# Kernel tuning notes

Measured on AMD Instinct MI355X. Metric: run time of the kernel, lower is better.

## Reference

```python
import jax, jax.numpy as jnp
import numpy as np

DIM = 1024
HEADS = 8
KV_HEADS = 1
GROUPS = HEADS // KV_HEADS
D_QK = 128
D_V = 192
DIM_PAIRWISE = 128
SCALE = 64 ** -0.5  # module uses dim_head=64 for scale, not dim_head_qk
SOFTCLAMP = 5.0
RMS_EPS = 1.1920929e-07  # torch nn.RMSNorm default eps = float32 machine eps
BN_EPS = 1e-05


def setup_inputs() -> dict:
    key = jax.random.key(0)
    ks = jax.random.split(key, 12)
    b, n, i = 1, 2048, 512
    qkv_out = HEADS * D_QK + D_QK + D_V  # 1344
    inv = lambda fan_in: 1.0 / np.sqrt(fan_in)
    return {
        "x": jax.random.normal(ks[0], (b, n, DIM), jnp.float32),
        "pairwise": jax.random.normal(ks[1], (b, i, i, DIM_PAIRWISE), jnp.float32),
        "rotary_emb": jax.random.normal(ks[2], (n, D_QK), jnp.float32),
        "W_qkv": jax.random.normal(ks[3], (DIM, qkv_out), jnp.float32) * inv(DIM),
        "q_norm_w": jnp.ones((D_QK,), jnp.float32),
        "k_norm_w": jnp.ones((D_QK,), jnp.float32),
        "v_norm_w": jnp.ones((D_V,), jnp.float32),
        "bn_gamma": jax.random.normal(ks[4], (DIM_PAIRWISE,), jnp.float32) * 0.02,
        "bn_beta": jax.random.normal(ks[5], (DIM_PAIRWISE,), jnp.float32) * 0.02,
        "bn_running_var": jnp.ones((DIM_PAIRWISE,), jnp.float32),
        "W_bias": jax.random.normal(ks[6], (DIM_PAIRWISE, HEADS), jnp.float32) * inv(DIM_PAIRWISE),
        "W_out": jax.random.normal(ks[7], (HEADS * D_V, DIM), jnp.float32) * inv(HEADS * D_V),
    }


def _rmsnorm(t, w):
    var = jnp.mean(jnp.square(t), axis=-1, keepdims=True)
    return t * jax.lax.rsqrt(var + RMS_EPS) * w


def _rotate_half(t):
    t1, t2 = jnp.split(t, 2, axis=-1)
    return jnp.concatenate((-t2, t1), axis=-1)


def _apply_rope(pos, t):
    return t * jnp.cos(pos) + _rotate_half(t) * jnp.sin(pos)


def reference(x, pairwise, rotary_emb, W_qkv, q_norm_w, k_norm_w, v_norm_w,
              bn_gamma, bn_beta, bn_running_var, W_bias, W_out):
    b, n, _ = x.shape
    qkv = x @ W_qkv
    q, k, v = jnp.split(qkv, [HEADS * D_QK, HEADS * D_QK + D_QK], axis=-1)

    # q: b n (g h d) -> b g h n d ; k,v: b n (h d) -> b h n d
    q = q.reshape(b, n, GROUPS, KV_HEADS, D_QK).transpose(0, 2, 3, 1, 4)
    k = k.reshape(b, n, KV_HEADS, D_QK).transpose(0, 2, 1, 3)
    v = v.reshape(b, n, KV_HEADS, D_V).transpose(0, 2, 1, 3)

    q = _rmsnorm(q, q_norm_w) * SCALE
    k = _rmsnorm(k, k_norm_w)
    v = _rmsnorm(v, v_norm_w)

    q = _apply_rope(rotary_emb, q)
    k = _apply_rope(rotary_emb, k)

    sim = jnp.einsum('bghid,bhjd->bghij', q, k)

    # pairwise attn bias: BatchRMSNorm (eval) -> GELU -> Linear -> b g h i j
    std = jnp.sqrt(jnp.clip(bn_running_var, BN_EPS, None))
    pw = pairwise / std * (DIM_PAIRWISE ** 0.5)
    pw = pw * (bn_gamma + 1.0) + bn_beta
    pw = jax.nn.gelu(pw, approximate=False)
    attn_bias = pw @ W_bias  # [b, i, j, heads]
    bi = attn_bias.shape[1]
    attn_bias = attn_bias.reshape(b, bi, bi, GROUPS, KV_HEADS).transpose(0, 3, 4, 1, 2)

    r = n // bi  # expand_factor
    attn_bias = jnp.repeat(jnp.repeat(attn_bias, r, axis=-2), r, axis=-1)

    sim = jnp.tanh((sim + attn_bias) / SOFTCLAMP) * SOFTCLAMP
    attn = jax.nn.softmax(sim, axis=-1)

    out = jnp.einsum('bghij,bhjd->bghid', attn, v)
    out = out.transpose(0, 3, 1, 2, 4).reshape(b, n, GROUPS * KV_HEADS * D_V)
    return out @ W_out
```

## Files before the change

kernel.cpp:

```cpp
#include <hip/hip_runtime.h>
#include <math.h>

typedef unsigned short u16;
typedef __attribute__((ext_vector_type(4))) float f32x4;
typedef __attribute__((ext_vector_type(8))) short s16x8;
typedef __attribute__((ext_vector_type(8))) _Float16 f16x8;

__device__ __forceinline__ u16 f2bf(float f){
  unsigned u = __builtin_bit_cast(unsigned, f);
  u += 0x7fffu + ((u >> 16) & 1u);
  return (u16)(u >> 16);
}
__device__ __forceinline__ float bf2f(u16 h){
  unsigned u = ((unsigned)h) << 16;
  return __builtin_bit_cast(float, u);
}
__device__ __forceinline__ u16 f2h(float f){
  return __builtin_bit_cast(u16, (_Float16)f);
}
__device__ __forceinline__ float h2f(u16 h){
  return (float)__builtin_bit_cast(_Float16, h);
}
__device__ __forceinline__ f32x4 mfma16(s16x8 a, s16x8 b, f32x4 c){
  return __builtin_amdgcn_mfma_f32_16x16x32_bf16(a, b, c, 0, 0, 0);
}
__device__ __forceinline__ f32x4 mfma16h(f16x8 a, f16x8 b, f32x4 c){
  return __builtin_amdgcn_mfma_f32_16x16x32_f16(a, b, c, 0, 0, 0);
}
__device__ __forceinline__ void gload16(const void* src, const u16* ldsbase){
  __builtin_amdgcn_global_load_lds(
      (const __attribute__((address_space(1))) void*)src,
      (__attribute__((address_space(3))) void*)ldsbase, 16, 0, 0);
}

__global__ __launch_bounds__(256) void k_pre(const float* __restrict__ x,
    const float* __restrict__ Wq, const float* __restrict__ Wo,
    u16* __restrict__ Afq, u16* __restrict__ Bq1, u16* __restrict__ Bq2){
  __shared__ float tile[64][65];
  int b = blockIdx.x, t = threadIdx.x;
  if (b < 1024){
    int id = b*256 + t;
    int row = id>>7, k0 = (id&127)*8;
    const float4* xp = (const float4*)(x + (size_t)row*1024 + k0);
    float4 v0 = xp[0], v1 = xp[1];
    float vv[8] = {v0.x,v0.y,v0.z,v0.w, v1.x,v1.y,v1.z,v1.w};
    u16 hh[8];
    #pragma unroll
    for (int e=0; e<8; ++e) hh[e] = f2h(vv[e]);
    int mt = row>>7, ms = (row>>4)&7, m16 = row&15;
    int kt = k0>>6, ks2 = (k0>>5)&1, lg = (k0>>3)&3;
    int lane = lg*16 + m16;
    size_t base = (size_t)(mt*16 + kt)*8192;
    *(uint4*)&Afq[base + (size_t)(ks2*8 + ms)*512 + lane*8] = *(uint4*)hh;
    return;
  }
  const float* in; u16* Bfq; int N, nKt, nt, kt;
  if (b < 1360){
    int bb = b - 1024; nt = bb % 21; kt = bb / 21;
    in = Wq; Bfq = Bq1; N = 1344; nKt = 16;
  } else {
    int bb = b - 1360; nt = bb % 16; kt = bb / 16;
    in = Wo; Bfq = Bq2; N = 1024; nKt = 24;
  }
  #pragma unroll
  for (int i=0; i<16; ++i){
    int idx = i*256 + t;
    int r = idx>>6, c = idx&63;
    tile[r][c] = in[(size_t)(kt*64 + r)*N + nt*64 + c];
  }
  __syncthreads();
  size_t base = (size_t)(nt*nKt + kt)*4096;
  #pragma unroll
  for (int j=0; j<2; ++j){
    int idx = j*256 + t;
    int np = idx>>3, ko = idx&7;
    u16 hh[8];
    #pragma unroll
    for (int e=0; e<8; ++e) hh[e] = f2h(tile[ko*8+e][np]);
    int ks2 = ko>>2, lg = ko&3, ns = np>>4, n16 = np&15;
    int lane = lg*16 + n16;
    *(uint4*)&Bfq[base + (size_t)(ks2*4 + ns)*512 + lane*8] = *(uint4*)hh;
  }
}

__global__ __launch_bounds__(256,3) void k_g1b(const u16* __restrict__ Afq,
    const u16* __restrict__ Bq1, u16* __restrict__ qkvh,
    const float* __restrict__ pw, const float* __restrict__ rv,
    const float* __restrict__ gamma, const float* __restrict__ beta,
    const float* __restrict__ Wb, float* __restrict__ bias){
  __shared__ u16 lds[24576];
  int b = blockIdx.x, t = threadIdx.x;
  int w = t>>6, lane = t&63, lg = lane>>4, lr = lane&15;
  if (b < 336){
    int id2 = (b & 7)*42 + (b >> 3);
    int by = id2 / 21, bx = id2 - by*21;
    int iw = w&1, jw = w>>1;
    int n0 = bx*64, m0 = by*128;
    const char* srcA = (const char*)(Afq + (size_t)by*16*8192);
    const char* srcB = (const char*)(Bq1 + (size_t)bx*16*4096);
    int wb = w*1024 + lane*16;
    auto stage = [&](int kt, int cur){
      const char* ta = srcA + (size_t)kt*16384;
      const char* tb = srcB + (size_t)kt*8192;
      int ab = cur*12288;
      #pragma unroll
      for (int i=0; i<4; ++i)
        gload16(ta + i*4096 + wb, &lds[ab + ((i*4096 + w*1024)>>1)]);
      #pragma unroll
      for (int i=0; i<2; ++i)
        gload16(tb + i*4096 + wb, &lds[ab + 8192 + ((i*4096 + w*1024)>>1)]);
    };
    f32x4 acc[4][2] = {};
    stage(0, 0);
    __syncthreads();
    int cur = 0;
    for (int kt=0; kt<16; ++kt){
      if (kt+1 < 16) stage(kt+1, cur^1);
      int ab = cur*12288;
      #pragma unroll
      for (int ks2=0; ks2<2; ++ks2){
        f16x8 ah[4], bh[2];
        #pragma unroll
        for (int m=0; m<4; ++m)
          ah[m] = *(const f16x8*)&lds[ab + (size_t)(ks2*8 + iw*4 + m)*512 + lane*8];
        #pragma unroll
        for (int n=0; n<2; ++n)
          bh[n] = *(const f16x8*)&lds[ab + 8192 + (size_t)(ks2*4 + jw*2 + n)*512 + lane*8];
        #pragma unroll
        for (int m=0; m<4; ++m)
          #pragma unroll
          for (int n=0; n<2; ++n)
            acc[m][n] = mfma16h(ah[m], bh[n], acc[m][n]);
      }
      __syncthreads();
      cur ^= 1;
    }
    #pragma unroll
    for (int m=0; m<4; ++m)
      #pragma unroll
      for (int n=0; n<2; ++n)
        #pragma unroll
        for (int r=0; r<4; ++r){
          int row = m0 + iw*64 + m*16 + lg*4 + r;
          int col = n0 + jw*32 + n*16 + lr;
          qkvh[(size_t)row*1344 + col] = f2h(acc[m][n][r]);
        }
    return;
  }
  int bb = b - 336;
  float* As = (float*)lds;
  float* Bs = As + 128;
  if (t < 128){
    As[t] = 11.313708498984761f * rsqrtf(fmaxf(rv[t], 1e-5f)) * (gamma[t] + 1.0f);
    Bs[t] = beta[t];
  }
  __syncthreads();
  s16x8 wbh[4], wbl[4];
  #pragma unroll
  for (int ks=0; ks<4; ++ks){
    s16x8 vh, vl;
    #pragma unroll
    for (int e=0; e<8; ++e){
      float v = (lr < 8) ? Wb[(ks*32 + lg*8 + e)*8 + lr] : 0.0f;
      u16 hh = f2bf(v);
      vh[e] = (short)hh;
      vl[e] = (short)f2bf(v - bf2f(hh));
    }
    wbh[ks] = vh; wbl[ks] = vl;
  }
  #pragma unroll
  for (int it=0; it<2; ++it){
    int p0 = bb*128 + it*64 + w*16;
    const float* rowp = pw + (size_t)(p0 + lr)*128;
    f32x4 acc = {0.f,0.f,0.f,0.f};
    #pragma unroll
    for (int ks=0; ks<4; ++ks){
      int c = ks*32 + lg*8;
      float4 x0 = *(const float4*)(rowp + c);
      float4 x1 = *(const float4*)(rowp + c + 4);
      float4 a0 = *(const float4*)&As[c], a1 = *(const float4*)&As[c+4];
      float4 b0 = *(const float4*)&Bs[c], b1 = *(const float4*)&Bs[c+4];
      float xv[8] = {x0.x*a0.x+b0.x, x0.y*a0.y+b0.y, x0.z*a0.z+b0.z, x0.w*a0.w+b0.w,
                     x1.x*a1.x+b1.x, x1.y*a1.y+b1.y, x1.z*a1.z+b1.z, x1.w*a1.w+b1.w};
      s16x8 gh, gl;
      #pragma unroll
      for (int e=0; e<8; ++e){
        float v = xv[e];
        float z = v * 0.7071067811865476f;
        float s = fabsf(z);
        float tt = 1.0f / (1.0f + 0.3275911f*s);
        float poly = ((((1.061405429f*tt - 1.453152027f)*tt + 1.421413741f)*tt - 0.284496736f)*tt + 0.254829592f)*tt;
        float E = __expf(-s*s);
        float Q = 0.5f*v*poly*E;
        float ge = (v >= 0.0f) ? (v - Q) : Q;
        u16 hh = f2bf(ge);
        gh[e] = (short)hh;
        gl[e] = (short)f2bf(ge - bf2f(hh));
      }
      acc = mfma16(gh, wbh[ks], acc);
      acc = mfma16(gh, wbl[ks], acc);
      acc = mfma16(gl, wbh[ks], acc);
    }
    if (lr < 8)
      #pragma unroll
      for (int r=0; r<4; ++r)
        bias[(size_t)(p0 + lg*4 + r)*8 + lr] = acc[r];
  }
}

__global__ __launch_bounds__(256) void k_norm(const u16* __restrict__ qkvh,
   const float* __restrict__ rot, const float* __restrict__ qw, const float* __restrict__ kw,
   const float* __restrict__ vw, u16* __restrict__ Qf, u16* __restrict__ KVF){
  int t = threadIdx.x;
  int w = t>>6, l = t&63;
  int task = blockIdx.x*4 + w;
  int n = task/10, g = task - (task/10)*10;
  const u16* row = qkvh + (size_t)n*1344;
  size_t tbase = (size_t)(n>>5)*10240;
  if (g < 9){
    float e0 = h2f(row[g*128 + l]);
    float e1 = h2f(row[g*128 + 64 + l]);
    float s = e0*e0 + e1*e1;
    #pragma unroll
    for (int m=1; m<64; m<<=1) s += __shfl_xor(s, m, 64);
    float rr = rsqrtf(s*(1.0f/128.0f) + 1.1920929e-07f);
    const float* ww = (g < 8) ? qw : kw;
    float sc = (g < 8) ? 0.125f : 1.0f;
    float qn0 = e0*rr*ww[l]*sc;
    float qn1 = e1*rr*ww[64+l]*sc;
    float p0 = rot[(size_t)n*128 + l], p1 = rot[(size_t)n*128 + 64 + l];
    float c0, s0, c1, s1;
    __sincosf(p0, &s0, &c0);
    __sincosf(p1, &s1, &c1);
    float o0 = qn0*c0 - qn1*s0;
    float o1 = qn1*c1 + qn0*s1;
    if (g < 8){
      Qf[((size_t)g*2048 + n)*128 + l]      = f2h(o0);
      Qf[((size_t)g*2048 + n)*128 + 64 + l] = f2h(o1);
    } else {
      int d0 = l, d1 = 64 + l;
      size_t ka0 = tbase + (size_t)((d0>>5)*2 + ((n>>4)&1))*512
                 + (size_t)(((d0>>3)&3)*16 + (n&15))*8 + (d0&7);
      size_t ka1 = tbase + (size_t)((d1>>5)*2 + ((n>>4)&1))*512
                 + (size_t)(((d1>>3)&3)*16 + (n&15))*8 + (d1&7);
      KVF[ka0] = f2h(o0);
      KVF[ka1] = f2h(o1);
    }
  } else {
    float v0 = h2f(row[1152 + l]);
    float v1 = h2f(row[1152 + 64 + l]);
    float v2 = h2f(row[1152 + 128 + l]);
    float s = v0*v0 + v1*v1 + v2*v2;
    #pragma unroll
    for (int m=1; m<64; m<<=1) s += __shfl_xor(s, m, 64);
    float rr = rsqrtf(s*(1.0f/192.0f) + 1.1920929e-07f);
    int lgv = (n>>3)&3, ev = n&7;
    size_t vbase = tbase + 4096;
    float vals[3] = {v0, v1, v2};
    #pragma unroll
    for (int j=0; j<3; ++j){
      int d = j*64 + l;
      KVF[vbase + (size_t)(d>>4)*512 + (size_t)(lgv*16 + (d&15))*8 + ev]
          = f2h(vals[j]*rr*vw[d]);
    }
  }
}

__global__ __launch_bounds__(256,3) void k_gemm2(const u16* __restrict__ Afq,
    const u16* __restrict__ Bfq, void* __restrict__ Cv, int N, int nKt, int halfOut, int NX){
  __shared__ u16 lds[24576];
  int id = blockIdx.x;
  int per = gridDim.x >> 3;
  int id2 = (id & 7)*per + (id >> 3);
  int by = id2 / NX;
  int bx = id2 - by*NX;
  int t = threadIdx.x;
  int w = t>>6, lane = t&63, lg = lane>>4, lr = lane&15;
  int iw = w&1, jw = w>>1;
  int n0 = bx*64, m0 = by*128;
  const char* srcA = (const char*)(Afq + (size_t)by*nKt*8192);
  const char* srcB = (const char*)(Bfq + (size_t)bx*nKt*4096);
  int wb = w*1024 + lane*16;
  auto stage = [&](int kt, int cur){
    const char* ta = srcA + (size_t)kt*16384;
    const char* tb = srcB + (size_t)kt*8192;
    int ab = cur*12288;
    #pragma unroll
    for (int i=0; i<4; ++i)
      gload16(ta + i*4096 + wb, &lds[ab + ((i*4096 + w*1024)>>1)]);
    #pragma unroll
    for (int i=0; i<2; ++i)
      gload16(tb + i*4096 + wb, &lds[ab + 8192 + ((i*4096 + w*1024)>>1)]);
  };
  f32x4 acc[4][2] = {};
  stage(0, 0);
  __syncthreads();
  int cur = 0;
  for (int kt=0; kt<nKt; ++kt){
    if (kt+1 < nKt) stage(kt+1, cur^1);
    int ab = cur*12288;
    #pragma unroll
    for (int ks2=0; ks2<2; ++ks2){
      f16x8 ah[4], bh[2];
      #pragma unroll
      for (int m=0; m<4; ++m)
        ah[m] = *(const f16x8*)&lds[ab + (size_t)(ks2*8 + iw*4 + m)*512 + lane*8];
      #pragma unroll
      for (int n=0; n<2; ++n)
        bh[n] = *(const f16x8*)&lds[ab + 8192 + (size_t)(ks2*4 + jw*2 + n)*512 + lane*8];
      #pragma unroll
      for (int m=0; m<4; ++m)
        #pragma unroll
        for (int n=0; n<2; ++n)
          acc[m][n] = mfma16h(ah[m], bh[n], acc[m][n]);
    }
    __syncthreads();
    cur ^= 1;
  }
  #pragma unroll
  for (int m=0; m<4; ++m)
    #pragma unroll
    for (int n=0; n<2; ++n)
      #pragma unroll
      for (int r=0; r<4; ++r){
        int row = m0 + iw*64 + m*16 + lg*4 + r;
        int col = n0 + jw*32 + n*16 + lr;
        if (halfOut) ((u16*)Cv)[(size_t)row*N + col] = f2h(acc[m][n][r]);
        else         ((float*)Cv)[(size_t)row*N + col] = acc[m][n][r];
      }
}

__global__ __launch_bounds__(256,2) void k_attn6(const u16* __restrict__ Qf,
  const u16* __restrict__ KVF, const float* __restrict__ bias,
  u16* __restrict__ OP, float* __restrict__ SP){
  __shared__ u16 lds[24576];
  int t = threadIdx.x;
  int w = t>>6, lane = t&63, lg = lane>>4, lr = lane&15;
  int q0 = blockIdx.x*32;
  int h  = blockIdx.y*4 + w;
  int zi = blockIdx.z;
  f16x8 qf[2][4];
  #pragma unroll
  for (int qi=0; qi<2; ++qi){
    const u16* qb = Qf + ((size_t)h*2048 + q0 + qi*16 + lr)*128 + lg*8;
    #pragma unroll
    for (int ks=0; ks<4; ++ks) qf[qi][ks] = *(const f16x8*)(qb + ks*32);
  }
  const char* kvb = (const char*)KVF + (size_t)zi*16*20480;
  int wb = w*1024 + lane*16;
  auto stage = [&](int jt, int cur){
    const char* src = kvb + (size_t)jt*20480;
    gload16(src + wb,         &lds[cur*4096 + (w*1024>>1)]);
    gload16(src + 4096 + wb,  &lds[cur*4096 + 2048 + (w*1024>>1)]);
    gload16(src + 8192 + wb,  &lds[8192 + cur*6144 + (w*1024>>1)]);
    gload16(src + 12288 + wb, &lds[8192 + cur*6144 + 2048 + (w*1024>>1)]);
    gload16(src + 16384 + wb, &lds[8192 + cur*6144 + 4096 + (w*1024>>1)]);
  };
  float bCur[2][2], bNxt[2][2];
  auto loadBias = [&](int jt, float bb[2][2]){
    int jq = (zi*512 + jt*32)>>2;
    #pragma unroll
    for (int qi=0; qi<2; ++qi)
      #pragma unroll
      for (int kj=0; kj<2; ++kj)
        bb[qi][kj] = bias[((size_t)((q0>>2) + qi*4 + lg)*512 + jq + kj*4 + (lr>>2))*8 + h];
  };
  stage(0, 0);
  loadBias(0, bCur);
  __syncthreads();
  f32x4 accO[2][12] = {};
  f32x4 accR[2] = {};
  f16x8 vone;
  #pragma unroll
  for (int e=0; e<8; ++e) vone[e] = (_Float16)1.0f;
  int psb = 20480 + w*1024;
  int po0 = lane*8;       po0 ^= ((po0>>6)&7)<<3;
  int po1 = 512 + lane*8; po1 ^= ((po1>>6)&7)<<3;
  int cur = 0;
  for (int jt=0; jt<16; ++jt){
    if (jt < 15){ stage(jt+1, cur^1); loadBias(jt+1, bNxt); }
    f32x4 accS[2][2] = {};
    #pragma unroll
    for (int ks=0; ks<4; ++ks){
      #pragma unroll
      for (int kj=0; kj<2; ++kj){
        f16x8 kb = *(const f16x8*)&lds[cur*4096 + (ks*2+kj)*512 + lane*8];
        accS[0][kj] = mfma16h(qf[0][ks], kb, accS[0][kj]);
        accS[1][kj] = mfma16h(qf[1][ks], kb, accS[1][kj]);
      }
    }
    #pragma unroll
    for (int qi=0; qi<2; ++qi)
      #pragma unroll
      for (int kj=0; kj<2; ++kj){
        float bv = bCur[qi][kj];
        #pragma unroll
        for (int r=0; r<4; ++r){
          float s = accS[qi][kj][r] + bv;
          float te = __expf(0.4f*s);
          float ri; asm("v_rcp_f32 %0, %1" : "=v"(ri) : "v"(te + 1.0f));
          float p = __expf(-10.0f*ri);
          int o = qi*512 + ((kj*2 + (lr>>3))*16 + lg*4 + r)*8 + (lr&7);
          o ^= ((o>>6)&7)<<3;
          lds[psb + o] = f2h(p);
        }
      }
    f16x8 pa0 = *(const f16x8*)&lds[psb + po0];
    f16x8 pa1 = *(const f16x8*)&lds[psb + po1];
    #pragma unroll
    for (int df=0; df<12; ++df){
      f16x8 vb = *(const f16x8*)&lds[8192 + cur*6144 + df*512 + lane*8];
      accO[0][df] = mfma16h(pa0, vb, accO[0][df]);
      accO[1][df] = mfma16h(pa1, vb, accO[1][df]);
    }
    accR[0] = mfma16h(pa0, vone, accR[0]);
    accR[1] = mfma16h(pa1, vone, accR[1]);
    __syncthreads();
    cur ^= 1;
    #pragma unroll
    for (int qi=0; qi<2; ++qi){ bCur[qi][0] = bNxt[qi][0]; bCur[qi][1] = bNxt[qi][1]; }
  }
  #pragma unroll
  for (int qi=0; qi<2; ++qi){
    #pragma unroll
    for (int df=0; df<12; ++df)
      #pragma unroll
      for (int r=0; r<4; ++r){
        int q = q0 + qi*16 + lg*4 + r;
        OP[(((size_t)zi*8 + h)*2048 + q)*192 + df*16 + lr] = f2h(accO[qi][df][r]);
      }
    if (lr == 0)
      #pragma unroll
      for (int r=0; r<4; ++r)
        SP[((size_t)zi*8 + h)*2048 + q0 + qi*16 + lg*4 + r] = accR[qi][r];
  }
}

__global__ __launch_bounds__(256) void k_comb2(const u16* __restrict__ OP,
    const float* __restrict__ SP, u16* __restrict__ Ao2){
  int id = blockIdx.x*256 + threadIdx.x;
  int hq = id / 24;
  int oct = id - hq*24;
  int d0 = oct*8;
  float inv = 1.0f / (SP[hq] + SP[16384+hq] + SP[32768+hq] + SP[49152+hq]);
  float o[8] = {0,0,0,0,0,0,0,0};
  #pragma unroll
  for (int z=0; z<4; ++z){
    uint4 v = *(const uint4*)&OP[((size_t)z*16384 + hq)*192 + d0];
    const u16* pv = (const u16*)&v;
    #pragma unroll
    for (int e=0; e<8; ++e) o[e] += h2f(pv[e]);
  }
  int h = hq >> 11, q = hq & 2047;
  int col = h*192 + d0;
  int kt = col>>6, ks2 = (col>>5)&1, lg = (col>>3)&3;
  int mt = q>>7, ms = (q>>4)&7, m16 = q&15;
  int lane = lg*16 + m16;
  u16 hh[8];
  #pragma unroll
  for (int e=0; e<8; ++e) hh[e] = f2h(o[e]*inv);
  size_t base = (size_t)(mt*24 + kt)*8192;
  *(uint4*)&Ao2[base + (size_t)(ks2*8 + ms)*512 + lane*8] = *(uint4*)hh;
}

extern "C" void kernel_launch(void* const* d_in, const int* in_sizes, int n_in,
                              void* d_out, int out_size, void* d_ws, size_t ws_size,
                              hipStream_t stream){
  (void)in_sizes; (void)n_in; (void)out_size; (void)ws_size;
  const float* x   = (const float*)d_in[0];
  const float* pwi = (const float*)d_in[1];
  const float* rot = (const float*)d_in[2];
  const float* Wq  = (const float*)d_in[3];
  const float* qw  = (const float*)d_in[4];
  const float* kw  = (const float*)d_in[5];
  const float* vw  = (const float*)d_in[6];
  const float* gm  = (const float*)d_in[7];
  const float* bt  = (const float*)d_in[8];
  const float* rvv = (const float*)d_in[9];
  const float* Wb  = (const float*)d_in[10];
  const float* Wo  = (const float*)d_in[11];
  float* out = (float*)d_out;
  char* ws = (char*)d_ws;
  size_t off = 0;
  auto alloc = [&](size_t bytes)->char*{
    char* p = ws + off; off = (off + bytes + 255) & ~(size_t)255; return p;
  };
  u16*   Axq = (u16*)alloc(16ull*16*8192*2);
  u16*   Bq1 = (u16*)alloc(21ull*16*4096*2);
  u16*   Bq2 = (u16*)alloc(16ull*24*4096*2);
  u16*   Ao2 = (u16*)alloc(16ull*24*8192*2);
  u16*   qkvh = (u16*)alloc(2048ull*1344*2);
  u16*   Qfb = (u16*)alloc(8ull*2048*128*2);
  u16*   KVF = (u16*)alloc(64ull*10240*2);
  float* bias = (float*)alloc(8ull*512*512*4);
  u16*   OP  = (u16*)alloc(4ull*8*2048*192*2);
  float* SP  = (float*)alloc(4ull*8*2048*4);

  k_pre<<<1744, 256, 0, stream>>>(x, Wq, Wo, Axq, Bq1, Bq2);
  k_g1b<<<2384, 256, 0, stream>>>(Axq, Bq1, qkvh, pwi, rvv, gm, bt, Wb, bias);
  k_norm<<<5120, 256, 0, stream>>>(qkvh, rot, qw, kw, vw, Qfb, KVF);
  k_attn6<<<dim3(64, 2, 4), 256, 0, stream>>>(Qfb, KVF, bias, OP, SP);
  k_comb2<<<1536, 256, 0, stream>>>(OP, SP, Ao2);
  k_gemm2<<<256, 256, 0, stream>>>(Ao2, Bq2, out, 1024, 24, 0, 16);
}
```

Measured before the change: 130.3 us.

## Use single fp16 MFMA for pairwise bias and store bias as fp16

Replaces the three-MFMA bf16 split-precision product in the pairwise bias path with one fp16 MFMA, and stores the bias tensor as fp16 instead of fp32, halving its memory traffic. The attention kernel now folds the 0.4 softclamp scale into the bias at load time, and its launch bounds are raised to allow three blocks per SIMD. Precision of the bias drops, and the higher occupancy target may force register spills in the attention kernel.

```diff
diff --git a/kernel.cpp b/kernel.cpp
--- a/kernel.cpp
+++ b/kernel.cpp
@@ -20,9 +20,6 @@
 }
 __device__ __forceinline__ float h2f(u16 h){
   return (float)__builtin_bit_cast(_Float16, h);
-}
-__device__ __forceinline__ f32x4 mfma16(s16x8 a, s16x8 b, f32x4 c){
-  return __builtin_amdgcn_mfma_f32_16x16x32_bf16(a, b, c, 0, 0, 0);
 }
 __device__ __forceinline__ f32x4 mfma16h(f16x8 a, f16x8 b, f32x4 c){
   return __builtin_amdgcn_mfma_f32_16x16x32_f16(a, b, c, 0, 0, 0);
@@ -87,7 +84,7 @@
     const u16* __restrict__ Bq1, u16* __restrict__ qkvh,
     const float* __restrict__ pw, const float* __restrict__ rv,
     const float* __restrict__ gamma, const float* __restrict__ beta,
-    const float* __restrict__ Wb, float* __restrict__ bias){
+    const float* __restrict__ Wb, u16* __restrict__ biash){
   __shared__ u16 lds[24576];
   int b = blockIdx.x, t = threadIdx.x;
   int w = t>>6, lane = t&63, lg = lane>>4, lr = lane&15;
@@ -155,18 +152,16 @@
     Bs[t] = beta[t];
   }
   __syncthreads();
-  s16x8 wbh[4], wbl[4];
+  f16x8 wbf[4];
   #pragma unroll
   for (int ks=0; ks<4; ++ks){
-    s16x8 vh, vl;
+    f16x8 vh;
     #pragma unroll
     for (int e=0; e<8; ++e){
       float v = (lr < 8) ? Wb[(ks*32 + lg*8 + e)*8 + lr] : 0.0f;
-      u16 hh = f2bf(v);
-      vh[e] = (short)hh;
-      vl[e] = (short)f2bf(v - bf2f(hh));
-    }
-    wbh[ks] = vh; wbl[ks] = vl;
+      vh[e] = (_Float16)v;
+    }
+    wbf[ks] = vh;
   }
   #pragma unroll
   for (int it=0; it<2; ++it){
@@ -182,7 +177,7 @@
       float4 b0 = *(const float4*)&Bs[c], b1 = *(const float4*)&Bs[c+4];
       float xv[8] = {x0.x*a0.x+b0.x, x0.y*a0.y+b0.y, x0.z*a0.z+b0.z, x0.w*a0.w+b0.w,
                      x1.x*a1.x+b1.x, x1.y*a1.y+b1.y, x1.z*a1.z+b1.z, x1.w*a1.w+b1.w};
-      s16x8 gh, gl;
+      f16x8 gh;
       #pragma unroll
       for (int e=0; e<8; ++e){
         float v = xv[e];
@@ -193,18 +188,14 @@
         float E = __expf(-s*s);
         float Q = 0.5f*v*poly*E;
         float ge = (v >= 0.0f) ? (v - Q) : Q;
-        u16 hh = f2bf(ge);
-        gh[e] = (short)hh;
-        gl[e] = (short)f2bf(ge - bf2f(hh));
-      }
-      acc = mfma16(gh, wbh[ks], acc);
-      acc = mfma16(gh, wbl[ks], acc);
-      acc = mfma16(gl, wbh[ks], acc);
+        gh[e] = (_Float16)ge;
+      }
+      acc = mfma16h(gh, wbf[ks], acc);
     }
     if (lr < 8)
       #pragma unroll
       for (int r=0; r<4; ++r)
-        bias[(size_t)(p0 + lg*4 + r)*8 + lr] = acc[r];
+        biash[(size_t)(p0 + lg*4 + r)*8 + lr] = f2h(acc[r]);
   }
 }
 
@@ -330,8 +321,8 @@
       }
 }
 
-__global__ __launch_bounds__(256,2) void k_attn6(const u16* __restrict__ Qf,
-  const u16* __restrict__ KVF, const float* __restrict__ bias,
+__global__ __launch_bounds__(256,3) void k_attn6(const u16* __restrict__ Qf,
+  const u16* __restrict__ KVF, const u16* __restrict__ biash,
   u16* __restrict__ OP, float* __restrict__ SP){
   __shared__ u16 lds[24576];
   int t = threadIdx.x;
@@ -363,7 +354,7 @@
     for (int qi=0; qi<2; ++qi)
       #pragma unroll
       for (int kj=0; kj<2; ++kj)
-        bb[qi][kj] = bias[((size_t)((q0>>2) + qi*4 + lg)*512 + jq + kj*4 + (lr>>2))*8 + h];
+        bb[qi][kj] = 0.4f*h2f(biash[((size_t)((q0>>2) + qi*4 + lg)*512 + jq + kj*4 + (lr>>2))*8 + h]);
   };
   stage(0, 0);
   loadBias(0, bCur);
@@ -396,8 +387,7 @@
         float bv = bCur[qi][kj];
         #pragma unroll
         for (int r=0; r<4; ++r){
-          float s = accS[qi][kj][r] + bv;
-          float te = __expf(0.4f*s);
+          float te = __expf(0.4f*accS[qi][kj][r] + bv);
           float ri; asm("v_rcp_f32 %0, %1" : "=v"(ri) : "v"(te + 1.0f));
           float p = __expf(-10.0f*ri);
           int o = qi*512 + ((kj*2 + (lr>>3))*16 + lg*4 + r)*8 + (lr&7);
@@ -492,14 +482,14 @@
   u16*   qkvh = (u16*)alloc(2048ull*1344*2);
   u16*   Qfb = (u16*)alloc(8ull*2048*128*2);
   u16*   KVF = (u16*)alloc(64ull*10240*2);
-  float* bias = (float*)alloc(8ull*512*512*4);
+  u16*   biash = (u16*)alloc(8ull*512*512*2);
   u16*   OP  = (u16*)alloc(4ull*8*2048*192*2);
   float* SP  = (float*)alloc(4ull*8*2048*4);
 
   k_pre<<<1744, 256, 0, stream>>>(x, Wq, Wo, Axq, Bq1, Bq2);
-  k_g1b<<<2384, 256, 0, stream>>>(Axq, Bq1, qkvh, pwi, rvv, gm, bt, Wb, bias);
+  k_g1b<<<2384, 256, 0, stream>>>(Axq, Bq1, qkvh, pwi, rvv, gm, bt, Wb, biash);
   k_norm<<<5120, 256, 0, stream>>>(qkvh, rot, qw, kw, vw, Qfb, KVF);
-  k_attn6<<<dim3(64, 2, 4), 256, 0, stream>>>(Qfb, KVF, bias, OP, SP);
+  k_attn6<<<dim3(64, 2, 4), 256, 0, stream>>>(Qfb, KVF, biash, OP, SP);
   k_comb2<<<1536, 256, 0, stream>>>(OP, SP, Ao2);
   k_gemm2<<<256, 256, 0, stream>>>(Ao2, Bq2, out, 1024, 24, 0, 16);
 }
```

Measured after the change: 170.7 us. 31.0% more time.
